# Kernel optimization log

Measured on AMD Instinct MI355X. Metric: run time of the kernel, lower is better.

## Reference

```python
import jax, jax.numpy as jnp
import numpy as np

T = 3          # frames
N = 2000       # num gaussians
H = 256
W = 256
DEG = 2        # polynomial_degree (opacity degree equal)
ALPHA_CLAMP = 0.999     # gsplat sum-rasterizer alpha clamp
ALPHA_THRESH = 1.0 / 255.0  # contributions below this are skipped by the kernel
CHOL_BOUND = jnp.array([0.5, 0.0, 0.5], dtype=jnp.float32)


def setup_inputs() -> dict:
    key = jax.random.key(0)
    k1, k2, k3, k4, k5, k6 = jax.random.split(key, 6)
    # xyz: c0 = atanh(2*(U-0.5)), higher-order coeffs small
    u = jax.random.uniform(k1, (1, N, 2), dtype=jnp.float32)
    c0_xyz = jnp.arctanh(jnp.clip(2.0 * (u - 0.5), -0.99, 0.99))
    hi_xyz = 0.1 * jax.random.normal(k2, (DEG, N, 2), dtype=jnp.float32)
    xyz_coeffs = jnp.concatenate([c0_xyz, hi_xyz], axis=0)
    # cholesky: c0 near [1,0,1] + noise, higher-order small
    c0_ch = jnp.array([1.0, 0.0, 1.0], dtype=jnp.float32)[None, None, :] \
        + 0.01 * jax.random.normal(k3, (1, N, 3), dtype=jnp.float32)
    hi_ch = 0.01 * jax.random.normal(k4, (DEG, N, 3), dtype=jnp.float32)
    cholesky_coeffs = jnp.concatenate([c0_ch, hi_ch], axis=0)
    # opacity: c0 = 0, small higher-order
    opacity_coeffs = jnp.concatenate(
        [jnp.zeros((1, N, 1), dtype=jnp.float32),
         0.05 * jax.random.normal(k5, (DEG, N, 1), dtype=jnp.float32)], axis=0)
    features_dc = jax.random.normal(k6, (N, 3), dtype=jnp.float32)
    return {"xyz_coeffs": xyz_coeffs, "cholesky_coeffs": cholesky_coeffs,
            "opacity_coeffs": opacity_coeffs, "features_dc": features_dc}


def _t_power_matrix(t):
    # [T, DEG+1]: columns 1, t, t^2, ...
    return jnp.stack([t ** d for d in range(DEG + 1)], axis=1)


def _render_frame(mx, my, conic, opac, colors):
    # mx,my: [N] pixel-space means; conic: [N,3] inverse-covariance (a,b,c); opac: [N]; colors: [N,3]
    xs = jnp.arange(W, dtype=jnp.float32)
    ys = jnp.arange(H, dtype=jnp.float32)
    dx = mx[:, None] - xs[None, :]          # [N, W]
    dy = my[:, None] - ys[None, :]          # [N, H]
    # Mahalanobis form q = a*dx^2 + 2b*dx*dy + c*dy^2  -> [N, H, W]
    q = (conic[:, 0:1, None] * (dx * dx)[:, None, :]
         + 2.0 * conic[:, 1:2, None] * dy[:, :, None] * dx[:, None, :]
         + conic[:, 2:3, None] * (dy * dy)[:, :, None])
    alpha = jnp.minimum(ALPHA_CLAMP, opac[:, None, None] * jnp.exp(-0.5 * q))
    alpha = jnp.where(alpha < ALPHA_THRESH, 0.0, alpha)  # kernel skips tiny contributions
    img = jnp.einsum('nhw,nc->hwc', alpha, colors)       # order-independent alpha sum
    return jnp.clip(img, 0.0, 1.0)


def reference(xyz_coeffs, cholesky_coeffs, opacity_coeffs, features_dc):
    t = jnp.linspace(0.0, 1.0, T).astype(jnp.float32)
    tp = _t_power_matrix(t)                                         # [T, DEG+1]
    xyz = jnp.tanh(jnp.einsum('dnp,td->tnp', xyz_coeffs, tp))       # [T,N,2] in (-1,1)
    chol = jnp.einsum('dnp,td->tnp', cholesky_coeffs, tp) + CHOL_BOUND[None, None, :]
    opac = jax.nn.sigmoid(jnp.einsum('dnp,td->tnp', opacity_coeffs, tp))[..., 0]  # [T,N]
    colors = jax.nn.sigmoid(features_dc)                            # [N,3]
    # project to pixel space
    mx = 0.5 * W * (xyz[..., 0] + 1.0)                              # [T,N]
    my = 0.5 * H * (xyz[..., 1] + 1.0)
    # Sigma = L L^T with L = [[l1,0],[l2,l3]]; conic = Sigma^{-1}
    l1, l2, l3 = chol[..., 0], chol[..., 1], chol[..., 2]
    a = l1 * l1
    b = l1 * l2
    c = l2 * l2 + l3 * l3
    det = a * c - b * b                                             # = (l1*l3)^2
    conic = jnp.stack([c / det, -b / det, a / det], axis=-1)        # [T,N,3]
    frames = [_render_frame(mx[i], my[i], conic[i], opac[i], colors) for i in range(T)]
    img = jnp.stack(frames, axis=0)                                 # [T,H,W,3]
    return jnp.transpose(img, (0, 3, 1, 2))                         # [T,3,H,W]
```

## Files before the change

### kernel.cpp

```cpp
#include <hip/hip_runtime.h>
#include <hip/hip_bf16.h>


#define TFRAMES 3
#define NG      2000
#define HH      256
#define WW      256
#define ALPHA_THRESH (1.0f / 255.0f)
#define ALPHA_CLAMP  0.999f

__device__ __forceinline__ float sigmoidf_(float x) { return 1.0f / (1.0f + expf(-x)); }


__global__ void gs_preprocess(const float* __restrict__ xyz,
                              const float* __restrict__ chol,
                              const float* __restrict__ opc,
                              const float* __restrict__ feat,
                              float4* __restrict__ cull,
                              float4* __restrict__ g1,
                              float4* __restrict__ g2)
{
    int n = blockIdx.x * blockDim.x + threadIdx.x;
    if (n >= NG) return;

    float cxc[3], cyc[3], l1c[3], l2c[3], l3c[3], opcc[3];
#pragma unroll
    for (int d = 0; d < 3; ++d) {
        cxc[d]  = xyz[(d * NG + n) * 2 + 0];
        cyc[d]  = xyz[(d * NG + n) * 2 + 1];
        l1c[d]  = chol[(d * NG + n) * 3 + 0];
        l2c[d]  = chol[(d * NG + n) * 3 + 1];
        l3c[d]  = chol[(d * NG + n) * 3 + 2];
        opcc[d] = opc[d * NG + n];
    }
    float cr = sigmoidf_(feat[n * 3 + 0]);
    float cg = sigmoidf_(feat[n * 3 + 1]);
    float cb = sigmoidf_(feat[n * 3 + 2]);

#pragma unroll
    for (int t = 0; t < TFRAMES; ++t) {
        float tv = (float)t / (float)(TFRAMES - 1);
        float vx = fmaf(tv, fmaf(tv, cxc[2], cxc[1]), cxc[0]);
        float vy = fmaf(tv, fmaf(tv, cyc[2], cyc[1]), cyc[0]);
        float l1 = fmaf(tv, fmaf(tv, l1c[2], l1c[1]), l1c[0]) + 0.5f;
        float l2 = fmaf(tv, fmaf(tv, l2c[2], l2c[1]), l2c[0]);
        float l3 = fmaf(tv, fmaf(tv, l3c[2], l3c[1]), l3c[0]) + 0.5f;
        float po = fmaf(tv, fmaf(tv, opcc[2], opcc[1]), opcc[0]);

        float mx = 128.0f * (tanhf(vx) + 1.0f);
        float my = 128.0f * (tanhf(vy) + 1.0f);

        float a = l1 * l1;
        float b = l1 * l2;
        float c = l2 * l2 + l3 * l3;
        float det = a * c - b * b;
        float opa = sigmoidf_(po);

        float rx = -1.0e9f, ry = -1.0e9f;
        float A = 0.f, B = 0.f, C = 0.f;
        if (det > 0.0f && det < 3.0e38f) {
            float inv = 1.0f / det;
            A = c * inv;
            B = -b * inv;
            C = a * inv;
            float s = opa * 255.0f;
            if (s > 1.0f) {
                float qm  = 2.0f * logf(s);
                float qmc = fmaf(qm, 1.0001f, 1e-3f);
                rx = sqrtf(qmc * a);
                ry = sqrtf(qmc * c);
            }
        }
        int idx = t * NG + n;
        cull[idx] = make_float4(mx, my, rx, ry);
        g1[idx]   = make_float4(A, B, C, opa);
        g2[idx]   = make_float4(cr, cg, cb, 0.0f);
    }
}

__global__ __launch_bounds__(256) void gs_render(const float4* __restrict__ cull,
                                                 const float4* __restrict__ g1,
                                                 const float4* __restrict__ g2,
                                                 float* __restrict__ out)
{
    const int tid = threadIdx.x;
    const int tx  = tid & 15;
    const int ty  = tid >> 4;
    const int px  = (blockIdx.x << 4) + tx;
    const int py  = (blockIdx.y << 4) + ty;
    const int t   = blockIdx.z;
    const float tcx = (float)(blockIdx.x << 4) + 7.5f;
    const float tcy = (float)(blockIdx.y << 4) + 7.5f;

    __shared__ int    s_cnt;
    __shared__ float2 s_pos[256];
    __shared__ float4 s_A[256];
    __shared__ float4 s_C[256];

    const float4* __restrict__ cu = cull + t * NG;
    const float4* __restrict__ gA = g1   + t * NG;
    const float4* __restrict__ gC = g2   + t * NG;

    float accr = 0.f, accg = 0.f, accb = 0.f;
    const float fx = (float)px, fy = (float)py;

    for (int base = 0; base < NG; base += 256) {
        if (tid == 0) s_cnt = 0;
        __syncthreads();

        int g = base + tid;
        if (g < NG) {
            float4 c4 = cu[g];
            if (fabsf(c4.x - tcx) <= c4.z + 7.5f &&
                fabsf(c4.y - tcy) <= c4.w + 7.5f) {
                int k = atomicAdd(&s_cnt, 1);
                s_pos[k] = make_float2(c4.x, c4.y);
                s_A[k]   = gA[g];
                s_C[k]   = gC[g];
            }
        }
        __syncthreads();

        int cnt = s_cnt;
        for (int j = 0; j < cnt; ++j) {
            float2 p = s_pos[j];
            float4 A = s_A[j];
            float dx = p.x - fx;
            float dy = p.y - fy;
            float q = A.x * dx * dx + 2.0f * A.y * dx * dy + A.z * dy * dy;
            float alpha = fminf(ALPHA_CLAMP, A.w * expf(-0.5f * q));
            float w = (alpha >= ALPHA_THRESH) ? alpha : 0.0f;
            float4 col = s_C[j];
            accr = fmaf(w, col.x, accr);
            accg = fmaf(w, col.y, accg);
            accb = fmaf(w, col.z, accb);
        }
        __syncthreads();
    }

    size_t o = (size_t)t * 3 * HH * WW + (size_t)py * WW + px;
    out[o]                        = fminf(fmaxf(accr, 0.f), 1.f);
    out[o + (size_t)HH * WW]      = fminf(fmaxf(accg, 0.f), 1.f);
    out[o + (size_t)2 * HH * WW]  = fminf(fmaxf(accb, 0.f), 1.f);
}

extern "C" void kernel_launch(void* const* d_in, const int* in_sizes, int n_in,
                              void* d_out, int out_size, void* d_ws, size_t ws_size,
                              hipStream_t stream)
{
    const float* xyz  = (const float*)d_in[0];
    const float* chol = (const float*)d_in[1];
    const float* opc  = (const float*)d_in[2];
    const float* feat = (const float*)d_in[3];
    float* out = (float*)d_out;

    char* ws = (char*)d_ws;
    float4* cull = (float4*)(ws);
    float4* g1   = (float4*)(ws + (size_t)TFRAMES * NG * 16);
    float4* g2   = (float4*)(ws + (size_t)2 * TFRAMES * NG * 16);

    gs_preprocess<<<dim3((NG + 255) / 256), dim3(256), 0, stream>>>(
        xyz, chol, opc, feat, cull, g1, g2);

    gs_render<<<dim3(WW / 16, HH / 16, TFRAMES), dim3(256), 0, stream>>>(
        cull, g1, g2, out);
}
```

Baseline: 72.88 us.

## Bin gaussians into per-tile lists in preprocess instead of per-block culling

Preprocessing now computes each gaussian's pixel bounding box and appends its parameters to per-tile lists with global atomics. A new kernel zeroes the tile counters first. The render kernel then streams only its own tile's list instead of scanning and culling all gaussians in every block. This trades the repeated culling scan for global atomics, an extra launch, a large workspace, and preprocessing that may be serialised by hot atomics. Gaussians cover roughly 3 pixels or less, so each touches few tiles. Per-tile list order is nondeterministic, which makes the float summation order nondeterministic.

```diff
diff --git a/kernel.cpp b/kernel.cpp
--- a/kernel.cpp
+++ b/kernel.cpp
@@ -6,19 +6,32 @@
 #define NG      2000
 #define HH      256
 #define WW      256
+#define NTX     16
+#define NTILES  (NTX * NTX)
+#define LIST_CAP NG
 #define ALPHA_THRESH (1.0f / 255.0f)
 #define ALPHA_CLAMP  0.999f
 
 __device__ __forceinline__ float sigmoidf_(float x) { return 1.0f / (1.0f + expf(-x)); }
 
+#define OFF_LPOS 4096
+#define OFF_LA   (OFF_LPOS + (size_t)TFRAMES * NTILES * LIST_CAP * 8)
+#define OFF_LC   (OFF_LA   + (size_t)TFRAMES * NTILES * LIST_CAP * 16)
+
+__global__ void gs_zero(int* __restrict__ counters)
+{
+    int i = blockIdx.x * blockDim.x + threadIdx.x;
+    if (i < TFRAMES * NTILES) counters[i] = 0;
+}
 
 __global__ void gs_preprocess(const float* __restrict__ xyz,
                               const float* __restrict__ chol,
                               const float* __restrict__ opc,
                               const float* __restrict__ feat,
-                              float4* __restrict__ cull,
-                              float4* __restrict__ g1,
-                              float4* __restrict__ g2)
+                              int*    __restrict__ counters,
+                              float2* __restrict__ lpos,
+                              float4* __restrict__ lA,
+                              float4* __restrict__ lC)
 {
     int n = blockIdx.x * blockDim.x + threadIdx.x;
     if (n >= NG) return;
@@ -56,73 +69,71 @@
         float det = a * c - b * b;
         float opa = sigmoidf_(po);
 
-        float rx = -1.0e9f, ry = -1.0e9f;
-        float A = 0.f, B = 0.f, C = 0.f;
-        if (det > 0.0f && det < 3.0e38f) {
-            float inv = 1.0f / det;
-            A = c * inv;
-            B = -b * inv;
-            C = a * inv;
-            float s = opa * 255.0f;
-            if (s > 1.0f) {
-                float qm  = 2.0f * logf(s);
-                float qmc = fmaf(qm, 1.0001f, 1e-3f);
-                rx = sqrtf(qmc * a);
-                ry = sqrtf(qmc * c);
+        if (!(det > 0.0f && det < 3.0e38f)) continue;
+        float inv = 1.0f / det;
+        float A = c * inv, B = -b * inv, C = a * inv;
+
+        float s = opa * 255.0f;
+        if (!(s > 1.0f)) continue;
+        float qm  = 2.0f * logf(s);
+        float qmc = fmaf(qm, 1.0001f, 1e-3f);
+        float rx = sqrtf(qmc * a);
+        float ry = sqrtf(qmc * c);
+
+        int xlo = (int)floorf(mx - rx), xhi = (int)ceilf(mx + rx);
+        int ylo = (int)floorf(my - ry), yhi = (int)ceilf(my + ry);
+        if (xhi < 0 || xlo > WW - 1 || yhi < 0 || ylo > HH - 1) continue;
+        xlo = max(xlo, 0); xhi = min(xhi, WW - 1);
+        ylo = max(ylo, 0); yhi = min(yhi, HH - 1);
+        int tx0 = xlo >> 4, tx1 = xhi >> 4;
+        int ty0 = ylo >> 4, ty1 = yhi >> 4;
+
+        float2 pos = make_float2(mx, my);
+        float4 gA  = make_float4(A, B, C, opa);
+        float4 gC  = make_float4(cr, cg, cb, 0.0f);
+        for (int ty = ty0; ty <= ty1; ++ty) {
+            for (int tx = tx0; tx <= tx1; ++tx) {
+                int tile = t * NTILES + ty * NTX + tx;
+                int slot = atomicAdd(&counters[tile], 1);
+                size_t e = (size_t)tile * LIST_CAP + slot;
+                lpos[e] = pos;
+                lA[e]   = gA;
+                lC[e]   = gC;
             }
         }
-        int idx = t * NG + n;
-        cull[idx] = make_float4(mx, my, rx, ry);
-        g1[idx]   = make_float4(A, B, C, opa);
-        g2[idx]   = make_float4(cr, cg, cb, 0.0f);
     }
 }
 
-__global__ __launch_bounds__(256) void gs_render(const float4* __restrict__ cull,
-                                                 const float4* __restrict__ g1,
-                                                 const float4* __restrict__ g2,
+__global__ __launch_bounds__(256) void gs_render(const int*    __restrict__ counters,
+                                                 const float2* __restrict__ lpos,
+                                                 const float4* __restrict__ lA,
+                                                 const float4* __restrict__ lC,
                                                  float* __restrict__ out)
 {
     const int tid = threadIdx.x;
-    const int tx  = tid & 15;
-    const int ty  = tid >> 4;
-    const int px  = (blockIdx.x << 4) + tx;
-    const int py  = (blockIdx.y << 4) + ty;
+    const int px  = (blockIdx.x << 4) + (tid & 15);
+    const int py  = (blockIdx.y << 4) + (tid >> 4);
     const int t   = blockIdx.z;
-    const float tcx = (float)(blockIdx.x << 4) + 7.5f;
-    const float tcy = (float)(blockIdx.y << 4) + 7.5f;
+    const int tile = t * NTILES + blockIdx.y * NTX + blockIdx.x;
+    const size_t base = (size_t)tile * LIST_CAP;
 
-    __shared__ int    s_cnt;
     __shared__ float2 s_pos[256];
     __shared__ float4 s_A[256];
     __shared__ float4 s_C[256];
 
-    const float4* __restrict__ cu = cull + t * NG;
-    const float4* __restrict__ gA = g1   + t * NG;
-    const float4* __restrict__ gC = g2   + t * NG;
-
+    const int cnt = counters[tile];
     float accr = 0.f, accg = 0.f, accb = 0.f;
     const float fx = (float)px, fy = (float)py;
 
-    for (int base = 0; base < NG; base += 256) {
-        if (tid == 0) s_cnt = 0;
-        __syncthreads();
-
-        int g = base + tid;
-        if (g < NG) {
-            float4 c4 = cu[g];
-            if (fabsf(c4.x - tcx) <= c4.z + 7.5f &&
-                fabsf(c4.y - tcy) <= c4.w + 7.5f) {
-                int k = atomicAdd(&s_cnt, 1);
-                s_pos[k] = make_float2(c4.x, c4.y);
-                s_A[k]   = gA[g];
-                s_C[k]   = gC[g];
-            }
+    for (int b0 = 0; b0 < cnt; b0 += 256) {
+        int m = min(cnt - b0, 256);
+        if (tid < m) {
+            s_pos[tid] = lpos[base + b0 + tid];
+            s_A[tid]   = lA[base + b0 + tid];
+            s_C[tid]   = lC[base + b0 + tid];
         }
         __syncthreads();
-
-        int cnt = s_cnt;
-        for (int j = 0; j < cnt; ++j) {
+        for (int j = 0; j < m; ++j) {
             float2 p = s_pos[j];
             float4 A = s_A[j];
             float dx = p.x - fx;
@@ -155,13 +166,16 @@
     float* out = (float*)d_out;
 
     char* ws = (char*)d_ws;
-    float4* cull = (float4*)(ws);
-    float4* g1   = (float4*)(ws + (size_t)TFRAMES * NG * 16);
-    float4* g2   = (float4*)(ws + (size_t)2 * TFRAMES * NG * 16);
+    int*    counters = (int*)ws;
+    float2* lpos = (float2*)(ws + OFF_LPOS);
+    float4* lA   = (float4*)(ws + OFF_LA);
+    float4* lC   = (float4*)(ws + OFF_LC);
+
+    gs_zero<<<dim3((TFRAMES * NTILES + 255) / 256), dim3(256), 0, stream>>>(counters);
 
     gs_preprocess<<<dim3((NG + 255) / 256), dim3(256), 0, stream>>>(
-        xyz, chol, opc, feat, cull, g1, g2);
+        xyz, chol, opc, feat, counters, lpos, lA, lC);
 
     gs_render<<<dim3(WW / 16, HH / 16, TFRAMES), dim3(256), 0, stream>>>(
-        cull, g1, g2, out);
+        counters, lpos, lA, lC, out);
 }
```

Measured after the change: 79.44 us. +9.0%, slower.

## Fuse gaussian preprocessing into render kernel with tighter fixed-radius culling

Applied to the files above, without the earlier changes.

Removes the separate preprocess kernel and its workspace round trip. Each render block now recomputes the per-gaussian polynomial evaluation, tanh, sigmoid and conic for its frame while loading gaussians into shared memory. Culling switches to a fixed Mahalanobis bound (QMAX) and an exact tile-box overlap test, and the color sigmoid is evaluated only for gaussians that survive. In exchange every tile redundantly recomputes the per-gaussian math, and the fixed bound may cull slightly differently from the old opacity-dependent radius.

```diff
diff --git a/kernel.cpp b/kernel.cpp
--- a/kernel.cpp
+++ b/kernel.cpp
@@ -8,98 +8,31 @@
 #define WW      256
 #define ALPHA_THRESH (1.0f / 255.0f)
 #define ALPHA_CLAMP  0.999f
+#define QMAX 11.1f
 
 __device__ __forceinline__ float sigmoidf_(float x) { return 1.0f / (1.0f + expf(-x)); }
 
-
-__global__ void gs_preprocess(const float* __restrict__ xyz,
-                              const float* __restrict__ chol,
-                              const float* __restrict__ opc,
-                              const float* __restrict__ feat,
-                              float4* __restrict__ cull,
-                              float4* __restrict__ g1,
-                              float4* __restrict__ g2)
-{
-    int n = blockIdx.x * blockDim.x + threadIdx.x;
-    if (n >= NG) return;
-
-    float cxc[3], cyc[3], l1c[3], l2c[3], l3c[3], opcc[3];
-#pragma unroll
-    for (int d = 0; d < 3; ++d) {
-        cxc[d]  = xyz[(d * NG + n) * 2 + 0];
-        cyc[d]  = xyz[(d * NG + n) * 2 + 1];
-        l1c[d]  = chol[(d * NG + n) * 3 + 0];
-        l2c[d]  = chol[(d * NG + n) * 3 + 1];
-        l3c[d]  = chol[(d * NG + n) * 3 + 2];
-        opcc[d] = opc[d * NG + n];
-    }
-    float cr = sigmoidf_(feat[n * 3 + 0]);
-    float cg = sigmoidf_(feat[n * 3 + 1]);
-    float cb = sigmoidf_(feat[n * 3 + 2]);
-
-#pragma unroll
-    for (int t = 0; t < TFRAMES; ++t) {
-        float tv = (float)t / (float)(TFRAMES - 1);
-        float vx = fmaf(tv, fmaf(tv, cxc[2], cxc[1]), cxc[0]);
-        float vy = fmaf(tv, fmaf(tv, cyc[2], cyc[1]), cyc[0]);
-        float l1 = fmaf(tv, fmaf(tv, l1c[2], l1c[1]), l1c[0]) + 0.5f;
-        float l2 = fmaf(tv, fmaf(tv, l2c[2], l2c[1]), l2c[0]);
-        float l3 = fmaf(tv, fmaf(tv, l3c[2], l3c[1]), l3c[0]) + 0.5f;
-        float po = fmaf(tv, fmaf(tv, opcc[2], opcc[1]), opcc[0]);
-
-        float mx = 128.0f * (tanhf(vx) + 1.0f);
-        float my = 128.0f * (tanhf(vy) + 1.0f);
-
-        float a = l1 * l1;
-        float b = l1 * l2;
-        float c = l2 * l2 + l3 * l3;
-        float det = a * c - b * b;
-        float opa = sigmoidf_(po);
-
-        float rx = -1.0e9f, ry = -1.0e9f;
-        float A = 0.f, B = 0.f, C = 0.f;
-        if (det > 0.0f && det < 3.0e38f) {
-            float inv = 1.0f / det;
-            A = c * inv;
-            B = -b * inv;
-            C = a * inv;
-            float s = opa * 255.0f;
-            if (s > 1.0f) {
-                float qm  = 2.0f * logf(s);
-                float qmc = fmaf(qm, 1.0001f, 1e-3f);
-                rx = sqrtf(qmc * a);
-                ry = sqrtf(qmc * c);
-            }
-        }
-        int idx = t * NG + n;
-        cull[idx] = make_float4(mx, my, rx, ry);
-        g1[idx]   = make_float4(A, B, C, opa);
-        g2[idx]   = make_float4(cr, cg, cb, 0.0f);
-    }
-}
-
-__global__ __launch_bounds__(256) void gs_render(const float4* __restrict__ cull,
-                                                 const float4* __restrict__ g1,
-                                                 const float4* __restrict__ g2,
-                                                 float* __restrict__ out)
+__global__ __launch_bounds__(256) void gs_fused(const float* __restrict__ xyz,
+                                                const float* __restrict__ chol,
+                                                const float* __restrict__ opc,
+                                                const float* __restrict__ feat,
+                                                float* __restrict__ out)
 {
     const int tid = threadIdx.x;
-    const int tx  = tid & 15;
-    const int ty  = tid >> 4;
-    const int px  = (blockIdx.x << 4) + tx;
-    const int py  = (blockIdx.y << 4) + ty;
+    const int px  = (blockIdx.x << 4) + (tid & 15);
+    const int py  = (blockIdx.y << 4) + (tid >> 4);
     const int t   = blockIdx.z;
-    const float tcx = (float)(blockIdx.x << 4) + 7.5f;
-    const float tcy = (float)(blockIdx.y << 4) + 7.5f;
+    const float tv = 0.5f * (float)t;
+
+    const float bx0 = (float)(blockIdx.x << 4) - 0.01f;
+    const float bx1 = (float)(blockIdx.x << 4) + 15.01f;
+    const float by0 = (float)(blockIdx.y << 4) - 0.01f;
+    const float by1 = (float)(blockIdx.y << 4) + 15.01f;
 
     __shared__ int    s_cnt;
     __shared__ float2 s_pos[256];
     __shared__ float4 s_A[256];
     __shared__ float4 s_C[256];
-
-    const float4* __restrict__ cu = cull + t * NG;
-    const float4* __restrict__ gA = g1   + t * NG;
-    const float4* __restrict__ gC = g2   + t * NG;
 
     float accr = 0.f, accg = 0.f, accb = 0.f;
     const float fx = (float)px, fy = (float)py;
@@ -110,13 +43,40 @@
 
         int g = base + tid;
         if (g < NG) {
-            float4 c4 = cu[g];
-            if (fabsf(c4.x - tcx) <= c4.z + 7.5f &&
-                fabsf(c4.y - tcy) <= c4.w + 7.5f) {
+            float x0 = xyz[g * 2 + 0],            y0 = xyz[g * 2 + 1];
+            float x1 = xyz[(NG + g) * 2 + 0],     y1 = xyz[(NG + g) * 2 + 1];
+            float x2 = xyz[(2 * NG + g) * 2 + 0], y2 = xyz[(2 * NG + g) * 2 + 1];
+            float vx = fmaf(tv, fmaf(tv, x2, x1), x0);
+            float vy = fmaf(tv, fmaf(tv, y2, y1), y0);
+            float l1 = fmaf(tv, fmaf(tv, chol[(2 * NG + g) * 3 + 0], chol[(NG + g) * 3 + 0]), chol[g * 3 + 0]) + 0.5f;
+            float l2 = fmaf(tv, fmaf(tv, chol[(2 * NG + g) * 3 + 1], chol[(NG + g) * 3 + 1]), chol[g * 3 + 1]);
+            float l3 = fmaf(tv, fmaf(tv, chol[(2 * NG + g) * 3 + 2], chol[(NG + g) * 3 + 2]), chol[g * 3 + 2]) + 0.5f;
+            float po = fmaf(tv, fmaf(tv, opc[2 * NG + g], opc[NG + g]), opc[g]);
+
+            float mx = 128.0f * (tanhf(vx) + 1.0f);
+            float my = 128.0f * (tanhf(vy) + 1.0f);
+
+            float a = l1 * l1;
+            float b = l1 * l2;
+            float c = l2 * l2 + l3 * l3;
+            float det = a * c - b * b;
+            float opa = sigmoidf_(po);
+
+            bool ok = (det > 0.0f) && (det < 3.0e38f) && (opa * 255.0f > 1.0f);
+            if (ok) {
+                float rx = sqrtf(QMAX * a);
+                float ry = sqrtf(QMAX * c);
+                ok = (mx + rx >= bx0) && (mx - rx <= bx1) &&
+                     (my + ry >= by0) && (my - ry <= by1);
+            }
+            if (ok) {
+                float inv = 1.0f / det;
                 int k = atomicAdd(&s_cnt, 1);
-                s_pos[k] = make_float2(c4.x, c4.y);
-                s_A[k]   = gA[g];
-                s_C[k]   = gC[g];
+                s_pos[k] = make_float2(mx, my);
+                s_A[k]   = make_float4(c * inv, -b * inv, a * inv, opa);
+                s_C[k]   = make_float4(sigmoidf_(feat[g * 3 + 0]),
+                                       sigmoidf_(feat[g * 3 + 1]),
+                                       sigmoidf_(feat[g * 3 + 2]), 0.0f);
             }
         }
         __syncthreads();
@@ -154,14 +114,6 @@
     const float* feat = (const float*)d_in[3];
     float* out = (float*)d_out;
 
-    char* ws = (char*)d_ws;
-    float4* cull = (float4*)(ws);
-    float4* g1   = (float4*)(ws + (size_t)TFRAMES * NG * 16);
-    float4* g2   = (float4*)(ws + (size_t)2 * TFRAMES * NG * 16);
-
-    gs_preprocess<<<dim3((NG + 255) / 256), dim3(256), 0, stream>>>(
-        xyz, chol, opc, feat, cull, g1, g2);
-
-    gs_render<<<dim3(WW / 16, HH / 16, TFRAMES), dim3(256), 0, stream>>>(
-        cull, g1, g2, out);
+    gs_fused<<<dim3(WW / 16, HH / 16, TFRAMES), dim3(256), 0, stream>>>(
+        xyz, chol, opc, feat, out);
 }
```

New measurement: 76.99 us. +5.6%, slower.

## Cull all gaussians up front, then compact survivors into dense shared-memory batches

Applied to the files above, without the earlier changes.

The render kernel now culls all 2000 gaussians for a tile in one pass. Each thread collects up to 8 hits locally and reserves slots in a shared index list with a single atomic per thread. The survivor list is then processed in dense batches of 256, which removes the per-chunk sync/atomic overhead and the sparse 8-iteration outer loop. The cost is 8KB of extra shared memory and an indirect gather of gaussian data, with a slightly widened cull margin. Workspace offsets are also changed to fixed constants.

```diff
diff --git a/kernel.cpp b/kernel.cpp
--- a/kernel.cpp
+++ b/kernel.cpp
@@ -11,6 +11,8 @@
 
 __device__ __forceinline__ float sigmoidf_(float x) { return 1.0f / (1.0f + expf(-x)); }
 
+#define OFF_G1 98304
+#define OFF_G2 196608
 
 __global__ void gs_preprocess(const float* __restrict__ xyz,
                               const float* __restrict__ chol,
@@ -39,7 +41,7 @@
 
 #pragma unroll
     for (int t = 0; t < TFRAMES; ++t) {
-        float tv = (float)t / (float)(TFRAMES - 1);
+        float tv = 0.5f * (float)t;
         float vx = fmaf(tv, fmaf(tv, cxc[2], cxc[1]), cxc[0]);
         float vy = fmaf(tv, fmaf(tv, cyc[2], cyc[1]), cyc[0]);
         float l1 = fmaf(tv, fmaf(tv, l1c[2], l1c[1]), l1c[0]) + 0.5f;
@@ -60,9 +62,7 @@
         float A = 0.f, B = 0.f, C = 0.f;
         if (det > 0.0f && det < 3.0e38f) {
             float inv = 1.0f / det;
-            A = c * inv;
-            B = -b * inv;
-            C = a * inv;
+            A = c * inv; B = -b * inv; C = a * inv;
             float s = opa * 255.0f;
             if (s > 1.0f) {
                 float qm  = 2.0f * logf(s);
@@ -84,16 +84,15 @@
                                                  float* __restrict__ out)
 {
     const int tid = threadIdx.x;
-    const int tx  = tid & 15;
-    const int ty  = tid >> 4;
-    const int px  = (blockIdx.x << 4) + tx;
-    const int py  = (blockIdx.y << 4) + ty;
+    const int px  = (blockIdx.x << 4) + (tid & 15);
+    const int py  = (blockIdx.y << 4) + (tid >> 4);
     const int t   = blockIdx.z;
     const float tcx = (float)(blockIdx.x << 4) + 7.5f;
     const float tcy = (float)(blockIdx.y << 4) + 7.5f;
 
     __shared__ int    s_cnt;
-    __shared__ float2 s_pos[256];
+    __shared__ int    s_idx[2048];
+    __shared__ float4 s_P[256];
     __shared__ float4 s_A[256];
     __shared__ float4 s_C[256];
 
@@ -101,32 +100,43 @@
     const float4* __restrict__ gA = g1   + t * NG;
     const float4* __restrict__ gC = g2   + t * NG;
 
+    int loc[8];
+    int nl = 0;
+#pragma unroll
+    for (int i = 0; i < 8; ++i) {
+        int g = i * 256 + tid;
+        if (g < NG) {
+            float4 c4 = cu[g];
+            if (fabsf(c4.x - tcx) <= c4.z + 7.51f &&
+                fabsf(c4.y - tcy) <= c4.w + 7.51f)
+                loc[nl++] = g;
+        }
+    }
+
+    if (tid == 0) s_cnt = 0;
+    __syncthreads();
+    int slot = (nl > 0) ? atomicAdd(&s_cnt, nl) : 0;
+    for (int k = 0; k < nl; ++k) s_idx[slot + k] = loc[k];
+    __syncthreads();
+
+    const int cnt = s_cnt;
     float accr = 0.f, accg = 0.f, accb = 0.f;
     const float fx = (float)px, fy = (float)py;
 
-    for (int base = 0; base < NG; base += 256) {
-        if (tid == 0) s_cnt = 0;
-        __syncthreads();
-
-        int g = base + tid;
-        if (g < NG) {
-            float4 c4 = cu[g];
-            if (fabsf(c4.x - tcx) <= c4.z + 7.5f &&
-                fabsf(c4.y - tcy) <= c4.w + 7.5f) {
-                int k = atomicAdd(&s_cnt, 1);
-                s_pos[k] = make_float2(c4.x, c4.y);
-                s_A[k]   = gA[g];
-                s_C[k]   = gC[g];
-            }
+    for (int b0 = 0; b0 < cnt; b0 += 256) {
+        int m = min(cnt - b0, 256);
+        if (tid < m) {
+            int idx = s_idx[b0 + tid];
+            s_P[tid] = cu[idx];
+            s_A[tid] = gA[idx];
+            s_C[tid] = gC[idx];
         }
         __syncthreads();
-
-        int cnt = s_cnt;
-        for (int j = 0; j < cnt; ++j) {
-            float2 p = s_pos[j];
+        for (int j = 0; j < m; ++j) {
+            float4 P = s_P[j];
             float4 A = s_A[j];
-            float dx = p.x - fx;
-            float dy = p.y - fy;
+            float dx = P.x - fx;
+            float dy = P.y - fy;
             float q = A.x * dx * dx + 2.0f * A.y * dx * dy + A.z * dy * dy;
             float alpha = fminf(ALPHA_CLAMP, A.w * expf(-0.5f * q));
             float w = (alpha >= ALPHA_THRESH) ? alpha : 0.0f;
@@ -156,8 +166,8 @@
 
     char* ws = (char*)d_ws;
     float4* cull = (float4*)(ws);
-    float4* g1   = (float4*)(ws + (size_t)TFRAMES * NG * 16);
-    float4* g2   = (float4*)(ws + (size_t)2 * TFRAMES * NG * 16);
+    float4* g1   = (float4*)(ws + OFF_G1);
+    float4* g2   = (float4*)(ws + OFF_G2);
 
     gs_preprocess<<<dim3((NG + 255) / 256), dim3(256), 0, stream>>>(
         xyz, chol, opc, feat, cull, g1, g2);
```

Measured after the change: 74.76 us. 1.03x slower.
